# Kernel optimization log

Measured on AMD Instinct MI355X. Metric: run time of the kernel, lower is better.

The kernel has to match this reference:

```python
import jax, jax.numpy as jnp
import numpy as np

EPS = 1e-12  # layer_norm_eps

def _ln(h, g, b):
    m = jnp.mean(h, axis=-1, keepdims=True)
    v = jnp.var(h, axis=-1, keepdims=True)
    return (h - m) / jnp.sqrt(v + EPS) * g + b

def setup_inputs() -> dict:
    key = jax.random.key(0)
    B, L, C, N = 32, 512, 256, 16
    ks = jax.random.split(key, 8)
    f = jax.random.normal
    return {
        'query': f(ks[0], (B, L, C), jnp.float32),
        'x': f(ks[1], (B, L, C), jnp.float32),
        'offset': f(ks[2], (B, L, 2 * N), jnp.float32) * 0.1,
        'w1': f(ks[3], (L, L // 4), jnp.float32) * 0.02, 'b1': jnp.zeros((L // 4,), jnp.float32),
        'g1': jnp.ones((L // 4,), jnp.float32), 'bt1': jnp.zeros((L // 4,), jnp.float32),
        'w2': f(ks[4], (L // 4, L), jnp.float32) * 0.02, 'b2': jnp.zeros((L,), jnp.float32),
        'w3': f(ks[5], (C, C), jnp.float32) * 0.02, 'b3': jnp.zeros((C,), jnp.float32),
        'g3': jnp.ones((C,), jnp.float32), 'bt3': jnp.zeros((C,), jnp.float32),
        'w4': f(ks[6], (C, 2 * N), jnp.float32) * 0.02, 'b4': jnp.zeros((2 * N,), jnp.float32),
    }

def reference(query, x, offset, w1, b1, g1, bt1, w2, b2, w3, b3, g3, bt3, w4, b4):
    B, L, C = x.shape
    N = w4.shape[1] // 2
    # sample_layer: Linear over the sequence axis (query permuted to [B,C,L])
    q = jnp.swapaxes(query, 1, 2)                                        # [B,C,L]
    q = jax.nn.gelu(_ln(q @ w1 + b1, g1, bt1), approximate=False) @ w2 + b2
    q = jnp.swapaxes(q, 1, 2)                                            # [B,L,C]
    # adjust_layer over channels -> per-step 2N offsets, tanh * 0.02
    adj = jax.nn.gelu(_ln(q @ w3 + b3, g3, bt3), approximate=False) @ w4 + b4
    adj = jnp.tanh(adj) * 0.02                                           # [B,L,2N]
    local = (offset + adj).reshape(B, L, N, 2)
    # precomputed reference points (x-coord 0, y-coord depends on query step i)
    i = jnp.arange(L, dtype=x.dtype)
    n = jnp.arange(N, dtype=x.dtype) + 0.5
    ref_y = n[None, :] * 2.0 * (i[:, None] + 1e-9) / (N * L) - 1.0       # [L,N]
    ref = jnp.stack([jnp.zeros_like(ref_y), ref_y], axis=-1)             # [L,N,2]
    pos = jnp.tanh(local + ref[None])                                    # [B,L,N,2]
    # grid_sample equivalent: input [B*L, C, H=L, W=1], align_corners=True,
    # bilinear, zero padding. With W=1 the x-coordinate always maps to col 0,
    # so only pos[...,1] matters. Causal mask zeroes keys h > query step l
    # before sampling; since bilinear sampling is linear in the input, we mask
    # the two gathered taps instead of materializing the O(B*L*L*C) tensor.
    pix = (pos[..., 1] + 1.0) * 0.5 * (L - 1)                            # [B,L,N]
    i0f = jnp.floor(pix)
    frac = pix - i0f
    i0 = i0f.astype(jnp.int32)
    i1 = i0 + 1
    lpos = jnp.arange(L, dtype=jnp.int32)[None, :, None]
    v0 = (i0 >= 0) & (i0 < L) & (i0 <= lpos)
    v1 = (i1 >= 0) & (i1 < L) & (i1 <= lpos)
    c0 = jnp.clip(i0, 0, L - 1)
    c1 = jnp.clip(i1, 0, L - 1)
    bidx = jnp.arange(B)[:, None, None]
    val0 = x[bidx, c0]                                                   # [B,L,N,C]
    val1 = x[bidx, c1]                                                   # [B,L,N,C]
    w0 = jnp.where(v0, 1.0 - frac, 0.0)
    w1_ = jnp.where(v1, frac, 0.0)
    out = w0[..., None] * val0 + w1_[..., None] * val1                   # [B,L,N,C]
    return (out, offset, pos)
```

## Files before the change

kernel.cpp:

```cpp
#include <hip/hip_runtime.h>
#include <hip/hip_fp16.h>
#include <math.h>


typedef _Float16 f16;
typedef _Float16 f16x8 __attribute__((ext_vector_type(8)));
typedef float f32x4 __attribute__((ext_vector_type(4)));

#define ZERO4 f32x4{0.f, 0.f, 0.f, 0.f}

__device__ __forceinline__ float gelu_exact(float v) {
  return 0.5f * v * (1.0f + erff(v * 0.70710678118654752f));
}

__global__ __launch_bounds__(256) void k0_prep(
    const float* __restrict__ w1, const float* __restrict__ w2,
    const float* __restrict__ w3, const float* __restrict__ w4,
    const float* __restrict__ query,
    f16* __restrict__ w1T, f16* __restrict__ w2T,
    f16* __restrict__ w3T, f16* __restrict__ w4T, f16* __restrict__ qT) {
  __shared__ f16 tile[64][80];
  int blk = blockIdx.x;
  const int tid = threadIdx.x;
  if (blk < 52) {
    const float* in; f16* out; int R, Cc, tr, tc;
    if (blk < 16)      { in = w1; out = w1T; R = 512; Cc = 128; tr = blk >> 1; tc = blk & 1; }
    else if (blk < 32) { blk -= 16; in = w2; out = w2T; R = 128; Cc = 512; tr = blk >> 3; tc = blk & 7; }
    else if (blk < 48) { blk -= 32; in = w3; out = w3T; R = 256; Cc = 256; tr = blk >> 2; tc = blk & 3; }
    else               { blk -= 48; in = w4; out = w4T; R = 256; Cc = 32;  tr = blk;      tc = 0; }
    const int r0 = tr * 64, c0 = tc * 64;
    for (int id = tid; id < 4096; id += 256) {
      int rr = id >> 6, cc = id & 63;
      if (c0 + cc < Cc) tile[cc][rr] = (f16)in[(r0 + rr) * Cc + c0 + cc];
    }
    __syncthreads();
    for (int id = tid; id < 512; id += 256) {
      int cc = id >> 3, ch = id & 7;
      if (c0 + cc < Cc)
        *(f16x8*)(out + (c0 + cc) * R + r0 + ch * 8) = *(f16x8*)&tile[cc][ch * 8];
    }
  } else {
    blk -= 52;
    const int b = blk >> 5, t = blk & 31;
    const int l0 = (t >> 2) << 6, c0 = (t & 3) << 6;
    for (int id = tid; id < 4096; id += 256) {
      int rr = id >> 6, cc = id & 63;
      tile[cc][rr] = (f16)query[((b << 9) + l0 + rr) * 256 + c0 + cc];
    }
    __syncthreads();
    for (int id = tid; id < 512; id += 256) {
      int cc = id >> 3, ch = id & 7;
      *(f16x8*)(qT + ((b << 8) + c0 + cc) * 512 + l0 + ch * 8) = *(f16x8*)&tile[cc][ch * 8];
    }
  }
}

__global__ __launch_bounds__(256) void k12_sample(
    const f16* __restrict__ qT, const f16* __restrict__ w1T,
    const f16* __restrict__ w2T,
    const float* __restrict__ b1, const float* __restrict__ g1,
    const float* __restrict__ bt1, const float* __restrict__ b2,
    f16* __restrict__ qout) {
  __shared__ char pool[38912];
  const int tid = threadIdx.x;
  const int b = blockIdx.x >> 4;
  const int c0 = (blockIdx.x & 15) << 4;
  const int lane = tid & 63, w = tid >> 6;
  const int mrow = lane & 15, kg = lane >> 4;
  char* At = pool;
  char* Bt = pool + 2048;
  char* t1s = pool + 32768;
  float* sb2 = (float*)(pool + 36864);

  sb2[tid] = b2[tid];
  sb2[tid + 256] = b2[tid + 256];

  f32x4 acc[2] = {ZERO4, ZERO4};
  for (int s = 0; s < 8; ++s) {
    const int k0 = s << 6;
    if (tid < 128) {
      int r = tid >> 3, c = tid & 7;
      f16x8 v = *(const f16x8*)(qT + ((b << 8) + c0 + r) * 512 + k0 + c * 8);
      *(f16x8*)(At + r * 128 + ((c * 16) ^ ((r & 7) << 4))) = v;
    }
    for (int id = tid; id < 1024; id += 256) {
      int rj = id >> 3, c = id & 7;
      f16x8 v = *(const f16x8*)(w1T + rj * 512 + k0 + c * 8);
      *(f16x8*)(Bt + rj * 128 + ((c * 16) ^ ((rj & 7) << 4))) = v;
    }
    __syncthreads();
#pragma unroll
    for (int kk = 0; kk < 2; ++kk) {
      f16x8 a = *(const f16x8*)(At + mrow * 128 + (((kk << 6) + (kg << 4)) ^ ((mrow & 7) << 4)));
#pragma unroll
      for (int nf = 0; nf < 2; ++nf) {
        int rn = w * 32 + nf * 16 + mrow;
        f16x8 bfr = *(const f16x8*)(Bt + rn * 128 + (((kk << 6) + (kg << 4)) ^ ((rn & 7) << 4)));
        acc[nf] = __builtin_amdgcn_mfma_f32_16x16x32_f16(a, bfr, acc[nf], 0, 0, 0);
      }
    }
    __syncthreads();
  }
  float (*hs)[132] = (float(*)[132])pool;
#pragma unroll
  for (int nf = 0; nf < 2; ++nf)
#pragma unroll
    for (int i = 0; i < 4; ++i)
      hs[kg * 4 + i][w * 32 + nf * 16 + mrow] = acc[nf][i];
  __syncthreads();
  {
    const int r = tid >> 4, g = tid & 15;
    float s1 = 0.f, s2 = 0.f, vals[8];
#pragma unroll
    for (int jj = 0; jj < 8; ++jj) {
      int j = g * 8 + jj;
      float v = hs[r][j] + b1[j];
      vals[jj] = v; s1 += v; s2 += v * v;
    }
#pragma unroll
    for (int m = 1; m < 16; m <<= 1) { s1 += __shfl_xor(s1, m, 64); s2 += __shfl_xor(s2, m, 64); }
    const float mean = s1 * (1.f / 128.f);
    float var = fmaxf(s2 * (1.f / 128.f) - mean * mean, 0.f);
    const float rstd = rsqrtf(var + 1e-12f);
    f16 ov[8];
#pragma unroll
    for (int jj = 0; jj < 8; ++jj) {
      int j = g * 8 + jj;
      float v = (vals[jj] - mean) * rstd * g1[j] + bt1[j];
      ov[jj] = (f16)gelu_exact(v);
    }
    __syncthreads();
    *(f16x8*)(t1s + r * 256 + ((g * 16) ^ ((r & 7) << 4))) = *(f16x8*)ov;
  }
  __syncthreads();

  char* At2 = pool;
  for (int lc = 0; lc < 4; ++lc) {
    for (int id = tid; id < 2048; id += 256) {
      int r = id >> 4, c = id & 15;
      f16x8 v = *(const f16x8*)(w2T + (lc * 128 + r) * 128 + c * 8);
      *(f16x8*)(At2 + r * 256 + ((c * 16) ^ ((r & 7) << 4))) = v;
    }
    __syncthreads();
    f32x4 acc2[2] = {ZERO4, ZERO4};
#pragma unroll
    for (int ks = 0; ks < 4; ++ks) {
      f16x8 bfr = *(const f16x8*)(t1s + mrow * 256 + (((ks << 6) + (kg << 4)) ^ ((mrow & 7) << 4)));
#pragma unroll
      for (int mf = 0; mf < 2; ++mf) {
        int rm = w * 32 + mf * 16 + mrow;
        f16x8 a = *(const f16x8*)(At2 + rm * 256 + (((ks << 6) + (kg << 4)) ^ ((rm & 7) << 4)));
        acc2[mf] = __builtin_amdgcn_mfma_f32_16x16x32_f16(a, bfr, acc2[mf], 0, 0, 0);
      }
    }
#pragma unroll
    for (int mf = 0; mf < 2; ++mf)
#pragma unroll
      for (int i = 0; i < 4; ++i) {
        int l = lc * 128 + w * 32 + mf * 16 + kg * 4 + i;
        qout[((b << 9) + l) * 256 + c0 + mrow] = (f16)(acc2[mf][i] + sb2[l]);
      }
    __syncthreads();
  }
}

__global__ __launch_bounds__(256) void k3_adjust(
    const f16* __restrict__ qbuf, const f16* __restrict__ w3T,
    const float* __restrict__ b3, const float* __restrict__ g3,
    const float* __restrict__ bt3, const f16* __restrict__ w4T,
    const float* __restrict__ b4, const float* __restrict__ offset,
    float* __restrict__ off_out, float* __restrict__ pos_out) {
  __shared__ char pool[50176];
  __shared__ char w4t[32 * 512];
  __shared__ float sb3[256];
  const int tid = threadIdx.x;
  const int b = blockIdx.x >> 4;
  const int l0 = (blockIdx.x & 15) << 5;
  const int lane = tid & 63, w = tid >> 6;
  const int mh = w & 1, nh = w >> 1;
  const int mrow = lane & 15, kg = lane >> 4;
  char* At = pool;
  char* Bt = pool + 4096;

  for (int id = tid; id < 1024; id += 256) {
    int r = id >> 5, c = id & 31;
    f16x8 v = *(const f16x8*)(w4T + r * 256 + c * 8);
    *(f16x8*)(w4t + r * 512 + ((c * 16) ^ ((r & 7) << 4))) = v;
  }
  sb3[tid] = b3[tid];

  f32x4 acc[8] = {ZERO4, ZERO4, ZERO4, ZERO4, ZERO4, ZERO4, ZERO4, ZERO4};
  for (int s = 0; s < 4; ++s) {
    const int k0 = s << 6;
    {
      int r = tid >> 3, c = tid & 7;
      f16x8 v = *(const f16x8*)(qbuf + ((b << 9) + l0 + r) * 256 + k0 + c * 8);
      *(f16x8*)(At + r * 128 + ((c * 16) ^ ((r & 7) << 4))) = v;
    }
    for (int id = tid; id < 2048; id += 256) {
      int r = id >> 3, c = id & 7;
      f16x8 v = *(const f16x8*)(w3T + r * 256 + k0 + c * 8);
      *(f16x8*)(Bt + r * 128 + ((c * 16) ^ ((r & 7) << 4))) = v;
    }
    __syncthreads();
#pragma unroll
    for (int kk = 0; kk < 2; ++kk) {
      int arow = mh * 16 + mrow;
      f16x8 a = *(const f16x8*)(At + arow * 128 + (((kk << 6) + (kg << 4)) ^ ((arow & 7) << 4)));
#pragma unroll
      for (int nf = 0; nf < 8; ++nf) {
        int rn = nh * 128 + nf * 16 + mrow;
        f16x8 bfr = *(const f16x8*)(Bt + rn * 128 + (((kk << 6) + (kg << 4)) ^ ((rn & 7) << 4)));
        acc[nf] = __builtin_amdgcn_mfma_f32_16x16x32_f16(a, bfr, acc[nf], 0, 0, 0);
      }
    }
    __syncthreads();
  }
  float (*hs)[264] = (float(*)[264])pool;
  char* ts = pool + 33792;
#pragma unroll
  for (int nf = 0; nf < 8; ++nf) {
    int col = nh * 128 + nf * 16 + mrow;
    float bias = sb3[col];
#pragma unroll
    for (int i = 0; i < 4; ++i)
      hs[mh * 16 + kg * 4 + i][col] = acc[nf][i] + bias;
  }
  __syncthreads();
  for (int p = 0; p < 2; ++p) {
    const int r = p * 16 + (tid >> 4), g = tid & 15;
    float s1 = 0.f, s2 = 0.f, vals[16];
#pragma unroll
    for (int jj = 0; jj < 16; ++jj) {
      float v = hs[r][g * 16 + jj];
      vals[jj] = v; s1 += v; s2 += v * v;
    }
#pragma unroll
    for (int m = 1; m < 16; m <<= 1) { s1 += __shfl_xor(s1, m, 64); s2 += __shfl_xor(s2, m, 64); }
    const float mean = s1 * (1.f / 256.f);
    float var = fmaxf(s2 * (1.f / 256.f) - mean * mean, 0.f);
    const float rstd = rsqrtf(var + 1e-12f);
    f16 ov[16];
#pragma unroll
    for (int jj = 0; jj < 16; ++jj) {
      int kch = g * 16 + jj;
      float v = (vals[jj] - mean) * rstd * g3[kch] + bt3[kch];
      ov[jj] = (f16)gelu_exact(v);
    }
    *(f16x8*)(ts + r * 512 + ((g * 32) ^ ((r & 7) << 4))) = *(f16x8*)&ov[0];
    *(f16x8*)(ts + r * 512 + ((g * 32 + 16) ^ ((r & 7) << 4))) = *(f16x8*)&ov[8];
  }
  __syncthreads();
  const int mf = w & 1, n4 = w >> 1;
  f32x4 a4 = ZERO4;
#pragma unroll
  for (int ks = 0; ks < 8; ++ks) {
    int ar = mf * 16 + mrow;
    f16x8 a = *(const f16x8*)(ts + ar * 512 + (((ks << 6) + (kg << 4)) ^ ((ar & 7) << 4)));
    int br = n4 * 16 + mrow;
    f16x8 bb = *(const f16x8*)(w4t + br * 512 + (((ks << 6) + (kg << 4)) ^ ((br & 7) << 4)));
    a4 = __builtin_amdgcn_mfma_f32_16x16x32_f16(a, bb, a4, 0, 0, 0);
  }
  const int col = n4 * 16 + mrow;
#pragma unroll
  for (int i = 0; i < 4; ++i) {
    const int row = mf * 16 + kg * 4 + i;
    const int l = l0 + row;
    float adj = tanhf(a4[i] + b4[col]) * 0.02f;
    float padj = __shfl_xor(adj, 1, 64);
    if ((lane & 1) == 0) {
      const int n = col >> 1;
      const float2 offv = *(const float2*)(offset + (((b << 9) + l) << 5) + col);
      const float pos0v = tanhf(offv.x + adj);
      const float ref_y = ((float)n + 0.5f) * ((float)l + 1e-9f) * (1.0f / 4096.0f) - 1.0f;
      const float pos1v = tanhf(offv.y + padj + ref_y);
      *(float2*)(off_out + (((b << 9) + l) << 5) + col) = offv;
      *(float2*)(pos_out + (((b << 9) + l) << 5) + col) = make_float2(pos0v, pos1v);
    }
  }
}

__global__ __launch_bounds__(256) void k4_gather(
    const float* __restrict__ x, const float* __restrict__ pos,
    float* __restrict__ outbuf) {
  const unsigned u = blockIdx.x * 256u + threadIdx.x;
  const unsigned t_idx = u >> 6;
  const unsigned cj = u & 63;
  const int b = t_idx >> 13;
  const int l = (t_idx >> 4) & 511;
  const float pos1 = pos[t_idx * 2 + 1];
  const float pix = (pos1 + 1.0f) * 0.5f * 511.0f;
  const float i0f = floorf(pix);
  const int i0 = (int)i0f;
  const float frac = pix - i0f;
  const int i1 = i0 + 1;
  const bool v0 = (i0 >= 0) && (i0 < 512) && (i0 <= l);
  const bool v1 = (i1 >= 0) && (i1 < 512) && (i1 <= l);
  const int c0 = i0 < 0 ? 0 : (i0 > 511 ? 511 : i0);
  const int c1 = i1 < 0 ? 0 : (i1 > 511 ? 511 : i1);
  const float w0  = v0 ? (1.0f - frac) : 0.0f;
  const float w1v = v1 ? frac : 0.0f;
  const float4* x4 = (const float4*)x;
  const float4 va = x4[(unsigned)((b << 9) + c0) * 64u + cj];
  const float4 vb = x4[(unsigned)((b << 9) + c1) * 64u + cj];
  float4 o;
  o.x = w0 * va.x + w1v * vb.x;
  o.y = w0 * va.y + w1v * vb.y;
  o.z = w0 * va.z + w1v * vb.z;
  o.w = w0 * va.w + w1v * vb.w;
  ((float4*)outbuf)[u] = o;
}

extern "C" void kernel_launch(void* const* d_in, const int* in_sizes, int n_in,
                              void* d_out, int out_size, void* d_ws, size_t ws_size,
                              hipStream_t stream) {
  const float* query  = (const float*)d_in[0];
  const float* x      = (const float*)d_in[1];
  const float* offset = (const float*)d_in[2];
  const float* w1  = (const float*)d_in[3];
  const float* b1  = (const float*)d_in[4];
  const float* g1  = (const float*)d_in[5];
  const float* bt1 = (const float*)d_in[6];
  const float* w2  = (const float*)d_in[7];
  const float* b2  = (const float*)d_in[8];
  const float* w3  = (const float*)d_in[9];
  const float* b3  = (const float*)d_in[10];
  const float* g3  = (const float*)d_in[11];
  const float* bt3 = (const float*)d_in[12];
  const float* w4  = (const float*)d_in[13];
  const float* b4  = (const float*)d_in[14];

  float* out     = (float*)d_out;
  float* off_out = out + 67108864;
  float* pos_out = off_out + 524288;

  f16* w1T = (f16*)d_ws;
  f16* w2T = w1T + 65536;
  f16* w3T = w2T + 65536;
  f16* w4T = w3T + 65536;
  f16* qT  = w4T + 8192;
  f16* q   = qT + 4194304;

  k0_prep<<<1076, 256, 0, stream>>>(w1, w2, w3, w4, query, w1T, w2T, w3T, w4T, qT);
  k12_sample<<<512, 256, 0, stream>>>(qT, w1T, w2T, b1, g1, bt1, b2, q);
  k3_adjust<<<512, 256, 0, stream>>>(q, w3T, b3, g3, bt3, w4T, b4, offset,
                                     off_out, pos_out);
  k4_gather<<<65536, 256, 0, stream>>>(x, pos_out, out);
}
```

Baseline: 122.4 us.

## Fuse query transpose into sample kernel, prefetch tiles, grid-stride gather with nontemporal stores

The separate query transpose pass in the prep kernel is removed. The sample kernel now reads fp32 query directly and transposes it into shared memory, cutting the fp16 qT round trip through global memory. The GEMM stages in both MLP kernels prefetch the next K-tile into registers while the current one is computed. The adjust kernel moves to 16-row tiles and twice the blocks. The gather kernel becomes a grid-stride loop with nontemporal stores for the large output. The costs are scalar f16 shared-memory writes for the query transpose, higher register pressure, and idle waves in the final small GEMM.

```diff
diff --git a/kernel.cpp b/kernel.cpp
--- a/kernel.cpp
+++ b/kernel.cpp
@@ -16,47 +16,31 @@
 __global__ __launch_bounds__(256) void k0_prep(
     const float* __restrict__ w1, const float* __restrict__ w2,
     const float* __restrict__ w3, const float* __restrict__ w4,
-    const float* __restrict__ query,
     f16* __restrict__ w1T, f16* __restrict__ w2T,
-    f16* __restrict__ w3T, f16* __restrict__ w4T, f16* __restrict__ qT) {
+    f16* __restrict__ w3T, f16* __restrict__ w4T) {
   __shared__ f16 tile[64][80];
   int blk = blockIdx.x;
   const int tid = threadIdx.x;
-  if (blk < 52) {
-    const float* in; f16* out; int R, Cc, tr, tc;
-    if (blk < 16)      { in = w1; out = w1T; R = 512; Cc = 128; tr = blk >> 1; tc = blk & 1; }
-    else if (blk < 32) { blk -= 16; in = w2; out = w2T; R = 128; Cc = 512; tr = blk >> 3; tc = blk & 7; }
-    else if (blk < 48) { blk -= 32; in = w3; out = w3T; R = 256; Cc = 256; tr = blk >> 2; tc = blk & 3; }
-    else               { blk -= 48; in = w4; out = w4T; R = 256; Cc = 32;  tr = blk;      tc = 0; }
-    const int r0 = tr * 64, c0 = tc * 64;
-    for (int id = tid; id < 4096; id += 256) {
-      int rr = id >> 6, cc = id & 63;
-      if (c0 + cc < Cc) tile[cc][rr] = (f16)in[(r0 + rr) * Cc + c0 + cc];
-    }
-    __syncthreads();
-    for (int id = tid; id < 512; id += 256) {
-      int cc = id >> 3, ch = id & 7;
-      if (c0 + cc < Cc)
-        *(f16x8*)(out + (c0 + cc) * R + r0 + ch * 8) = *(f16x8*)&tile[cc][ch * 8];
-    }
-  } else {
-    blk -= 52;
-    const int b = blk >> 5, t = blk & 31;
-    const int l0 = (t >> 2) << 6, c0 = (t & 3) << 6;
-    for (int id = tid; id < 4096; id += 256) {
-      int rr = id >> 6, cc = id & 63;
-      tile[cc][rr] = (f16)query[((b << 9) + l0 + rr) * 256 + c0 + cc];
-    }
-    __syncthreads();
-    for (int id = tid; id < 512; id += 256) {
-      int cc = id >> 3, ch = id & 7;
-      *(f16x8*)(qT + ((b << 8) + c0 + cc) * 512 + l0 + ch * 8) = *(f16x8*)&tile[cc][ch * 8];
-    }
+  const float* in; f16* out; int R, Cc, tr, tc;
+  if (blk < 16)      { in = w1; out = w1T; R = 512; Cc = 128; tr = blk >> 1; tc = blk & 1; }
+  else if (blk < 32) { blk -= 16; in = w2; out = w2T; R = 128; Cc = 512; tr = blk >> 3; tc = blk & 7; }
+  else if (blk < 48) { blk -= 32; in = w3; out = w3T; R = 256; Cc = 256; tr = blk >> 2; tc = blk & 3; }
+  else               { blk -= 48; in = w4; out = w4T; R = 256; Cc = 32;  tr = blk;      tc = 0; }
+  const int r0 = tr * 64, c0 = tc * 64;
+  for (int id = tid; id < 4096; id += 256) {
+    int rr = id >> 6, cc = id & 63;
+    if (c0 + cc < Cc) tile[cc][rr] = (f16)in[(r0 + rr) * Cc + c0 + cc];
+  }
+  __syncthreads();
+  for (int id = tid; id < 512; id += 256) {
+    int cc = id >> 3, ch = id & 7;
+    if (c0 + cc < Cc)
+      *(f16x8*)(out + (c0 + cc) * R + r0 + ch * 8) = *(f16x8*)&tile[cc][ch * 8];
   }
 }
 
 __global__ __launch_bounds__(256) void k12_sample(
-    const f16* __restrict__ qT, const f16* __restrict__ w1T,
+    const float* __restrict__ query, const f16* __restrict__ w1T,
     const f16* __restrict__ w2T,
     const float* __restrict__ b1, const float* __restrict__ g1,
     const float* __restrict__ bt1, const float* __restrict__ b2,
@@ -75,20 +59,37 @@
   sb2[tid] = b2[tid];
   sb2[tid + 256] = b2[tid + 256];
 
+  const int qll = tid >> 4, qcc = tid & 15;
+  const int wrj = tid >> 3, wch = tid & 7;
+
+  float qv[4]; f16x8 wv[4];
+#pragma unroll
+  for (int it = 0; it < 4; ++it) {
+    qv[it] = query[(((b << 9) + 0 + qll + it * 16) << 8) + c0 + qcc];
+    wv[it] = *(const f16x8*)(w1T + (wrj + it * 32) * 512 + 0 + wch * 8);
+  }
+
   f32x4 acc[2] = {ZERO4, ZERO4};
   for (int s = 0; s < 8; ++s) {
-    const int k0 = s << 6;
-    if (tid < 128) {
-      int r = tid >> 3, c = tid & 7;
-      f16x8 v = *(const f16x8*)(qT + ((b << 8) + c0 + r) * 512 + k0 + c * 8);
-      *(f16x8*)(At + r * 128 + ((c * 16) ^ ((r & 7) << 4))) = v;
-    }
-    for (int id = tid; id < 1024; id += 256) {
-      int rj = id >> 3, c = id & 7;
-      f16x8 v = *(const f16x8*)(w1T + rj * 512 + k0 + c * 8);
-      *(f16x8*)(Bt + rj * 128 + ((c * 16) ^ ((rj & 7) << 4))) = v;
-    }
-    __syncthreads();
+#pragma unroll
+    for (int it = 0; it < 4; ++it) {
+      int ll = qll + it * 16;
+      *(f16*)(At + qcc * 128 + ((2 * ll) ^ ((qcc & 7) << 4))) = (f16)qv[it];
+    }
+#pragma unroll
+    for (int it = 0; it < 4; ++it) {
+      int rj = wrj + it * 32;
+      *(f16x8*)(Bt + rj * 128 + ((wch * 16) ^ ((rj & 7) << 4))) = wv[it];
+    }
+    __syncthreads();
+    if (s < 7) {
+      const int k0n = (s + 1) << 6;
+#pragma unroll
+      for (int it = 0; it < 4; ++it) {
+        qv[it] = query[(((b << 9) + k0n + qll + it * 16) << 8) + c0 + qcc];
+        wv[it] = *(const f16x8*)(w1T + (wrj + it * 32) * 512 + k0n + wch * 8);
+      }
+    }
 #pragma unroll
     for (int kk = 0; kk < 2; ++kk) {
       f16x8 a = *(const f16x8*)(At + mrow * 128 + (((kk << 6) + (kg << 4)) ^ ((mrow & 7) << 4)));
@@ -101,6 +102,12 @@
     }
     __syncthreads();
   }
+
+  f16x8 av[8];
+#pragma unroll
+  for (int it = 0; it < 8; ++it)
+    av[it] = *(const f16x8*)(w2T + ((tid >> 4) + it * 16) * 128 + (tid & 15) * 8);
+
   float (*hs)[132] = (float(*)[132])pool;
 #pragma unroll
   for (int nf = 0; nf < 2; ++nf)
@@ -135,13 +142,19 @@
   __syncthreads();
 
   char* At2 = pool;
+  const int ar2 = tid >> 4, ac2 = tid & 15;
   for (int lc = 0; lc < 4; ++lc) {
-    for (int id = tid; id < 2048; id += 256) {
-      int r = id >> 4, c = id & 15;
-      f16x8 v = *(const f16x8*)(w2T + (lc * 128 + r) * 128 + c * 8);
-      *(f16x8*)(At2 + r * 256 + ((c * 16) ^ ((r & 7) << 4))) = v;
-    }
-    __syncthreads();
+#pragma unroll
+    for (int it = 0; it < 8; ++it) {
+      int r = ar2 + it * 16;
+      *(f16x8*)(At2 + r * 256 + ((ac2 * 16) ^ ((r & 7) << 4))) = av[it];
+    }
+    __syncthreads();
+    if (lc < 3) {
+#pragma unroll
+      for (int it = 0; it < 8; ++it)
+        av[it] = *(const f16x8*)(w2T + ((lc + 1) * 128 + ar2 + it * 16) * 128 + ac2 * 8);
+    }
     f32x4 acc2[2] = {ZERO4, ZERO4};
 #pragma unroll
     for (int ks = 0; ks < 4; ++ks) {
@@ -170,17 +183,16 @@
     const float* __restrict__ bt3, const f16* __restrict__ w4T,
     const float* __restrict__ b4, const float* __restrict__ offset,
     float* __restrict__ off_out, float* __restrict__ pos_out) {
-  __shared__ char pool[50176];
+  __shared__ char pool[34816];
   __shared__ char w4t[32 * 512];
   __shared__ float sb3[256];
   const int tid = threadIdx.x;
-  const int b = blockIdx.x >> 4;
-  const int l0 = (blockIdx.x & 15) << 5;
+  const int b = blockIdx.x >> 5;
+  const int l0 = (blockIdx.x & 31) << 4;
   const int lane = tid & 63, w = tid >> 6;
-  const int mh = w & 1, nh = w >> 1;
   const int mrow = lane & 15, kg = lane >> 4;
   char* At = pool;
-  char* Bt = pool + 4096;
+  char* Bt = pool + 2048;
 
   for (int id = tid; id < 1024; id += 256) {
     int r = id >> 5, c = id & 31;
@@ -189,27 +201,36 @@
   }
   sb3[tid] = b3[tid];
 
-  f32x4 acc[8] = {ZERO4, ZERO4, ZERO4, ZERO4, ZERO4, ZERO4, ZERO4, ZERO4};
+  const int sr = tid >> 3, sc = tid & 7;
+  f16x8 aq; f16x8 bq[8];
+  if (tid < 128) aq = *(const f16x8*)(qbuf + ((b << 9) + l0 + sr) * 256 + 0 + sc * 8);
+#pragma unroll
+  for (int it = 0; it < 8; ++it)
+    bq[it] = *(const f16x8*)(w3T + (sr + it * 32) * 256 + 0 + sc * 8);
+
+  f32x4 acc[4] = {ZERO4, ZERO4, ZERO4, ZERO4};
   for (int s = 0; s < 4; ++s) {
-    const int k0 = s << 6;
-    {
-      int r = tid >> 3, c = tid & 7;
-      f16x8 v = *(const f16x8*)(qbuf + ((b << 9) + l0 + r) * 256 + k0 + c * 8);
-      *(f16x8*)(At + r * 128 + ((c * 16) ^ ((r & 7) << 4))) = v;
-    }
-    for (int id = tid; id < 2048; id += 256) {
-      int r = id >> 3, c = id & 7;
-      f16x8 v = *(const f16x8*)(w3T + r * 256 + k0 + c * 8);
-      *(f16x8*)(Bt + r * 128 + ((c * 16) ^ ((r & 7) << 4))) = v;
-    }
-    __syncthreads();
+    if (tid < 128)
+      *(f16x8*)(At + sr * 128 + ((sc * 16) ^ ((sr & 7) << 4))) = aq;
+#pragma unroll
+    for (int it = 0; it < 8; ++it) {
+      int r = sr + it * 32;
+      *(f16x8*)(Bt + r * 128 + ((sc * 16) ^ ((r & 7) << 4))) = bq[it];
+    }
+    __syncthreads();
+    if (s < 3) {
+      const int k0n = (s + 1) << 6;
+      if (tid < 128) aq = *(const f16x8*)(qbuf + ((b << 9) + l0 + sr) * 256 + k0n + sc * 8);
+#pragma unroll
+      for (int it = 0; it < 8; ++it)
+        bq[it] = *(const f16x8*)(w3T + (sr + it * 32) * 256 + k0n + sc * 8);
+    }
 #pragma unroll
     for (int kk = 0; kk < 2; ++kk) {
-      int arow = mh * 16 + mrow;
-      f16x8 a = *(const f16x8*)(At + arow * 128 + (((kk << 6) + (kg << 4)) ^ ((arow & 7) << 4)));
-#pragma unroll
-      for (int nf = 0; nf < 8; ++nf) {
-        int rn = nh * 128 + nf * 16 + mrow;
+      f16x8 a = *(const f16x8*)(At + mrow * 128 + (((kk << 6) + (kg << 4)) ^ ((mrow & 7) << 4)));
+#pragma unroll
+      for (int nf = 0; nf < 4; ++nf) {
+        int rn = w * 64 + nf * 16 + mrow;
         f16x8 bfr = *(const f16x8*)(Bt + rn * 128 + (((kk << 6) + (kg << 4)) ^ ((rn & 7) << 4)));
         acc[nf] = __builtin_amdgcn_mfma_f32_16x16x32_f16(a, bfr, acc[nf], 0, 0, 0);
       }
@@ -217,18 +238,18 @@
     __syncthreads();
   }
   float (*hs)[264] = (float(*)[264])pool;
-  char* ts = pool + 33792;
-#pragma unroll
-  for (int nf = 0; nf < 8; ++nf) {
-    int col = nh * 128 + nf * 16 + mrow;
+  char* ts = pool + 17408;
+#pragma unroll
+  for (int nf = 0; nf < 4; ++nf) {
+    int col = w * 64 + nf * 16 + mrow;
     float bias = sb3[col];
 #pragma unroll
     for (int i = 0; i < 4; ++i)
-      hs[mh * 16 + kg * 4 + i][col] = acc[nf][i] + bias;
-  }
-  __syncthreads();
-  for (int p = 0; p < 2; ++p) {
-    const int r = p * 16 + (tid >> 4), g = tid & 15;
+      hs[kg * 4 + i][col] = acc[nf][i] + bias;
+  }
+  __syncthreads();
+  {
+    const int r = tid >> 4, g = tid & 15;
     float s1 = 0.f, s2 = 0.f, vals[16];
 #pragma unroll
     for (int jj = 0; jj < 16; ++jj) {
@@ -251,31 +272,32 @@
     *(f16x8*)(ts + r * 512 + ((g * 32 + 16) ^ ((r & 7) << 4))) = *(f16x8*)&ov[8];
   }
   __syncthreads();
-  const int mf = w & 1, n4 = w >> 1;
-  f32x4 a4 = ZERO4;
-#pragma unroll
-  for (int ks = 0; ks < 8; ++ks) {
-    int ar = mf * 16 + mrow;
-    f16x8 a = *(const f16x8*)(ts + ar * 512 + (((ks << 6) + (kg << 4)) ^ ((ar & 7) << 4)));
-    int br = n4 * 16 + mrow;
-    f16x8 bb = *(const f16x8*)(w4t + br * 512 + (((ks << 6) + (kg << 4)) ^ ((br & 7) << 4)));
-    a4 = __builtin_amdgcn_mfma_f32_16x16x32_f16(a, bb, a4, 0, 0, 0);
-  }
-  const int col = n4 * 16 + mrow;
-#pragma unroll
-  for (int i = 0; i < 4; ++i) {
-    const int row = mf * 16 + kg * 4 + i;
-    const int l = l0 + row;
-    float adj = tanhf(a4[i] + b4[col]) * 0.02f;
-    float padj = __shfl_xor(adj, 1, 64);
-    if ((lane & 1) == 0) {
-      const int n = col >> 1;
-      const float2 offv = *(const float2*)(offset + (((b << 9) + l) << 5) + col);
-      const float pos0v = tanhf(offv.x + adj);
-      const float ref_y = ((float)n + 0.5f) * ((float)l + 1e-9f) * (1.0f / 4096.0f) - 1.0f;
-      const float pos1v = tanhf(offv.y + padj + ref_y);
-      *(float2*)(off_out + (((b << 9) + l) << 5) + col) = offv;
-      *(float2*)(pos_out + (((b << 9) + l) << 5) + col) = make_float2(pos0v, pos1v);
+  if (w < 2) {
+    const int n4 = w;
+    f32x4 a4 = ZERO4;
+#pragma unroll
+    for (int ks = 0; ks < 8; ++ks) {
+      f16x8 a = *(const f16x8*)(ts + mrow * 512 + (((ks << 6) + (kg << 4)) ^ ((mrow & 7) << 4)));
+      int br = n4 * 16 + mrow;
+      f16x8 bb = *(const f16x8*)(w4t + br * 512 + (((ks << 6) + (kg << 4)) ^ ((br & 7) << 4)));
+      a4 = __builtin_amdgcn_mfma_f32_16x16x32_f16(a, bb, a4, 0, 0, 0);
+    }
+    const int col = n4 * 16 + mrow;
+#pragma unroll
+    for (int i = 0; i < 4; ++i) {
+      const int row = kg * 4 + i;
+      const int l = l0 + row;
+      float adj = tanhf(a4[i] + b4[col]) * 0.02f;
+      float padj = __shfl_xor(adj, 1, 64);
+      if ((lane & 1) == 0) {
+        const int n = col >> 1;
+        const float2 offv = *(const float2*)(offset + (((b << 9) + l) << 5) + col);
+        const float pos0v = tanhf(offv.x + adj);
+        const float ref_y = ((float)n + 0.5f) * ((float)l + 1e-9f) * (1.0f / 4096.0f) - 1.0f;
+        const float pos1v = tanhf(offv.y + padj + ref_y);
+        *(float2*)(off_out + (((b << 9) + l) << 5) + col) = offv;
+        *(float2*)(pos_out + (((b << 9) + l) << 5) + col) = make_float2(pos0v, pos1v);
+      }
     }
   }
 }
@@ -283,32 +305,30 @@
 __global__ __launch_bounds__(256) void k4_gather(
     const float* __restrict__ x, const float* __restrict__ pos,
     float* __restrict__ outbuf) {
-  const unsigned u = blockIdx.x * 256u + threadIdx.x;
-  const unsigned t_idx = u >> 6;
-  const unsigned cj = u & 63;
-  const int b = t_idx >> 13;
-  const int l = (t_idx >> 4) & 511;
-  const float pos1 = pos[t_idx * 2 + 1];
-  const float pix = (pos1 + 1.0f) * 0.5f * 511.0f;
-  const float i0f = floorf(pix);
-  const int i0 = (int)i0f;
-  const float frac = pix - i0f;
-  const int i1 = i0 + 1;
-  const bool v0 = (i0 >= 0) && (i0 < 512) && (i0 <= l);
-  const bool v1 = (i1 >= 0) && (i1 < 512) && (i1 <= l);
-  const int c0 = i0 < 0 ? 0 : (i0 > 511 ? 511 : i0);
-  const int c1 = i1 < 0 ? 0 : (i1 > 511 ? 511 : i1);
-  const float w0  = v0 ? (1.0f - frac) : 0.0f;
-  const float w1v = v1 ? frac : 0.0f;
-  const float4* x4 = (const float4*)x;
-  const float4 va = x4[(unsigned)((b << 9) + c0) * 64u + cj];
-  const float4 vb = x4[(unsigned)((b << 9) + c1) * 64u + cj];
-  float4 o;
-  o.x = w0 * va.x + w1v * vb.x;
-  o.y = w0 * va.y + w1v * vb.y;
-  o.z = w0 * va.z + w1v * vb.z;
-  o.w = w0 * va.w + w1v * vb.w;
-  ((float4*)outbuf)[u] = o;
+  const unsigned tbase = blockIdx.x * 256u + threadIdx.x;
+  for (unsigned u = tbase; u < 16777216u; u += 524288u) {
+    const unsigned t_idx = u >> 6;
+    const unsigned cj = u & 63;
+    const int b = t_idx >> 13;
+    const int l = (t_idx >> 4) & 511;
+    const float pos1 = pos[t_idx * 2 + 1];
+    const float pix = (pos1 + 1.0f) * 0.5f * 511.0f;
+    const float i0f = floorf(pix);
+    const int i0 = (int)i0f;
+    const float frac = pix - i0f;
+    const int i1 = i0 + 1;
+    const bool v0 = (i0 >= 0) && (i0 < 512) && (i0 <= l);
+    const bool v1 = (i1 >= 0) && (i1 < 512) && (i1 <= l);
+    const int c0 = i0 < 0 ? 0 : (i0 > 511 ? 511 : i0);
+    const int c1 = i1 < 0 ? 0 : (i1 > 511 ? 511 : i1);
+    const float w0  = v0 ? (1.0f - frac) : 0.0f;
+    const float w1v = v1 ? frac : 0.0f;
+    const f32x4* x4 = (const f32x4*)x;
+    const f32x4 va = x4[(unsigned)((b << 9) + c0) * 64u + cj];
+    const f32x4 vb = x4[(unsigned)((b << 9) + c1) * 64u + cj];
+    f32x4 o = w0 * va + w1v * vb;
+    __builtin_nontemporal_store(o, (f32x4*)outbuf + u);
+  }
 }
 
 extern "C" void kernel_launch(void* const* d_in, const int* in_sizes, int n_in,
@@ -338,12 +358,11 @@
   f16* w2T = w1T + 65536;
   f16* w3T = w2T + 65536;
   f16* w4T = w3T + 65536;
-  f16* qT  = w4T + 8192;
-  f16* q   = qT + 4194304;
-
-  k0_prep<<<1076, 256, 0, stream>>>(w1, w2, w3, w4, query, w1T, w2T, w3T, w4T, qT);
-  k12_sample<<<512, 256, 0, stream>>>(qT, w1T, w2T, b1, g1, bt1, b2, q);
-  k3_adjust<<<512, 256, 0, stream>>>(q, w3T, b3, g3, bt3, w4T, b4, offset,
-                                     off_out, pos_out);
-  k4_gather<<<65536, 256, 0, stream>>>(x, pos_out, out);
-}
+  f16* q   = w4T + 8192;
+
+  k0_prep<<<52, 256, 0, stream>>>(w1, w2, w3, w4, w1T, w2T, w3T, w4T);
+  k12_sample<<<512, 256, 0, stream>>>(query, w1T, w2T, b1, g1, bt1, b2, q);
+  k3_adjust<<<1024, 256, 0, stream>>>(q, w3T, b3, g3, bt3, w4T, b4, offset,
+                                      off_out, pos_out);
+  k4_gather<<<2048, 256, 0, stream>>>(x, pos_out, out);
+}
```

Measured after the change: 114.4 us. 1.07x faster.
